# Performance work log

Hardware: AMD Instinct MI355X
Metric: run time of the kernel (lower is better)

Reference implementation:

```python
import jax, jax.numpy as jnp
import numpy as np

# Module hyperparameters (init_kwargs)
THRESHOLD_ABS = 0.2
THRESHOLD_REL = 0.05   # set to None to disable the relative-threshold branch
MIN_DISTANCE = 3


def setup_inputs() -> dict:
    key = jax.random.key(0)
    # belief maps in [0, 1), NCHW
    belive_map = jax.random.uniform(key, (32, 4, 512, 512), dtype=jnp.float32)
    return {"belive_map": belive_map}


def reference(belive_map):
    """Peak detection on belief maps (dense, jit-friendly form).

    Faithful to BeliveMapsNMS.forward: the torch module additionally compacts
    the mask into (coords, labels, scores) lists via nonzero/gather, which has
    data-dependent shapes; here we return the equivalent dense outputs:
      mask        [B,C,H,W] bool   - peak locations (nonzero of this == torch ind)
      scores_abs  [B,C,H,W] f32    - belief value at peaks, 0 elsewhere
      scores_rel  [B,C,H,W] f32    - scores_abs / per-(b,c) max
    """
    k = 2 * MIN_DISTANCE + 1          # 7
    pad = k // 2                       # 3 -> 'same' max pool, stride 1

    # F.max_pool2d(kernel=k, stride=1, padding=k//2)
    x_max = jax.lax.reduce_window(
        belive_map, -jnp.inf, jax.lax.max,
        window_dimensions=(1, 1, k, k),
        window_strides=(1, 1, 1, 1),
        padding=[(0, 0), (0, 0), (pad, pad), (pad, pad)],
    )

    # per-(batch, channel) global max: hh.max(dim=2) on the flattened map
    vmax = jnp.max(belive_map, axis=(2, 3), keepdims=True)  # [B,C,1,1]

    mask = (x_max == belive_map) & (belive_map > THRESHOLD_ABS)
    if THRESHOLD_REL is not None:
        mask = mask & (belive_map > THRESHOLD_REL * vmax)

    scores_abs = jnp.where(mask, belive_map, jnp.float32(0.0))
    scores_rel = scores_abs / vmax
    return mask, scores_abs, scores_rel
```

## Files before the change

### kernel.cpp

```cpp
#include <hip/hip_runtime.h>
#include <math.h>


#define H 512
#define W 512
#define PLANE_ELEMS (H * W)
#define TH 8
#define LROWS (TH + 6)
#define NEG_INF (-INFINITY)
#define VCHUNKS 16

typedef float v4f __attribute__((ext_vector_type(4)));

__device__ __forceinline__ float4 vmax4(float4 a, float4 b) {
    return make_float4(fmaxf(a.x, b.x), fmaxf(a.y, b.y), fmaxf(a.z, b.z), fmaxf(a.w, b.w));
}

__device__ __forceinline__ void nt_store4(float* p, float a, float b, float c, float d) {
    v4f v = {a, b, c, d};
    __builtin_nontemporal_store(v, (v4f*)p);
}

__global__ __launch_bounds__(256) void vmax_kernel(const float* __restrict__ in,
                                                   float* __restrict__ partials) {
    const int chunk = blockIdx.x;
    const int plane = blockIdx.y;
    const float4* p = (const float4*)(in + (size_t)plane * PLANE_ELEMS) + chunk * 4096;
    float4 v[16];
    #pragma unroll
    for (int j = 0; j < 16; ++j) v[j] = p[threadIdx.x + (j << 8)];
    float4 t[8];
    #pragma unroll
    for (int j = 0; j < 8; ++j) t[j] = vmax4(v[j], v[j + 8]);
    #pragma unroll
    for (int j = 0; j < 4; ++j) t[j] = vmax4(t[j], t[j + 4]);
    float4 q = vmax4(vmax4(t[0], t[1]), vmax4(t[2], t[3]));
    float m = fmaxf(fmaxf(q.x, q.y), fmaxf(q.z, q.w));
    #pragma unroll
    for (int o = 32; o > 0; o >>= 1) m = fmaxf(m, __shfl_down(m, o, 64));
    __shared__ float s[4];
    if ((threadIdx.x & 63) == 0) s[threadIdx.x >> 6] = m;
    __syncthreads();
    if (threadIdx.x == 0) {
        partials[(plane << 4) + chunk] = fmaxf(fmaxf(s[0], s[1]), fmaxf(s[2], s[3]));
    }
}

__global__ __launch_bounds__(256, 4) void nms_kernel(const float* __restrict__ in,
                                                     const float* __restrict__ partials,
                                                     float* __restrict__ out, int N) {
    const int hwid = blockIdx.x + (blockIdx.y << 6);
    const int wg = ((hwid & 7) << 10) + (hwid >> 3);
    const int plane = wg >> 6;
    const int ty0 = (wg & 63) * TH;

    const float* pin = in + (size_t)plane * PLANE_ELEMS;

    __shared__ __align__(16) float sRow[LROWS * W];

    const int wid = threadIdx.x >> 6;
    const int lane = threadIdx.x & 63;
    const int c8 = lane << 3;

    float pm[16];
    #pragma unroll
    for (int j = 0; j < 16; ++j) pm[j] = partials[(plane << 4) + j];

    float4 va[4], vb[4];
    #pragma unroll
    for (int k = 0; k < 4; ++k) {
        const int r = wid + (k << 2);
        if (r < LROWS) {
            const int gy = ty0 + r - 3;
            if (gy >= 0 && gy < H) {
                const float4* row = (const float4*)(pin + (size_t)gy * W);
                va[k] = row[lane * 2];
                vb[k] = row[lane * 2 + 1];
            } else {
                va[k] = vb[k] = make_float4(NEG_INF, NEG_INF, NEG_INF, NEG_INF);
            }
        }
    }

    #pragma unroll
    for (int k = 0; k < 4; ++k) {
        const int r = wid + (k << 2);
        if (r < LROWS) {
            float4 v0 = va[k], v1 = vb[k];
            float l0 = __shfl_up(v1.y, 1, 64), l1 = __shfl_up(v1.z, 1, 64), l2 = __shfl_up(v1.w, 1, 64);
            float r0 = __shfl_down(v0.x, 1, 64), r1 = __shfl_down(v0.y, 1, 64), r2 = __shfl_down(v0.z, 1, 64);
            if (lane == 0) { l0 = NEG_INF; l1 = NEG_INF; l2 = NEG_INF; }
            if (lane == 63) { r0 = NEG_INF; r1 = NEG_INF; r2 = NEG_INF; }
            float a[14] = {l0, l1, l2, v0.x, v0.y, v0.z, v0.w, v1.x, v1.y, v1.z, v1.w, r0, r1, r2};
            float A[7];
            A[6] = a[6];
            #pragma unroll
            for (int j = 5; j >= 0; --j) A[j] = fmaxf(a[j], A[j + 1]);
            float rm[8];
            rm[0] = A[0];
            float B = a[7];
            rm[1] = fmaxf(A[1], B);
            #pragma unroll
            for (int j = 2; j <= 6; ++j) { B = fmaxf(B, a[6 + j]); rm[j] = fmaxf(A[j], B); }
            B = fmaxf(B, a[13]);
            rm[7] = B;
            float4* dst = (float4*)&sRow[r * W + c8];
            dst[0] = make_float4(rm[0], rm[1], rm[2], rm[3]);
            dst[1] = make_float4(rm[4], rm[5], rm[6], rm[7]);
        }
    }

    const int strip = threadIdx.x >> 7;
    const int cg = threadIdx.x & 127;
    const int c = cg << 2;
    const int y0 = strip << 2;
    const int gy_base = ty0 + y0;

    float4 ctr[4];
    #pragma unroll
    for (int i = 0; i < 4; ++i) {
        ctr[i] = *(const float4*)(pin + (size_t)(gy_base + i) * W + c);
    }

    float vmax = pm[0];
    #pragma unroll
    for (int j = 1; j < 16; ++j) vmax = fmaxf(vmax, pm[j]);
    const float rel_thr = 0.05f * vmax;
    const float inv_vmax = 1.0f / vmax;

    __syncthreads();

    float* __restrict__ omask = out;
    float* __restrict__ oabs = out + (size_t)N;
    float* __restrict__ orel = out + 2 * (size_t)N;

    float4 Lr[7];
    #pragma unroll
    for (int k = 0; k < 7; ++k) Lr[k] = *(const float4*)&sRow[(y0 + k) * W + c];
    float4 Aq[4];
    {
        float4 suf = vmax4(Lr[4], vmax4(Lr[5], Lr[6]));
        Aq[3] = vmax4(Lr[3], suf);
        Aq[2] = vmax4(Lr[2], Aq[3]);
        Aq[1] = vmax4(Lr[1], Aq[2]);
        Aq[0] = vmax4(Lr[0], Aq[1]);
    }

    float4 Bq;
    #pragma unroll
    for (int i = 0; i < 4; ++i) {
        float4 m;
        if (i == 0) {
            m = Aq[0];
        } else {
            float4 row = *(const float4*)&sRow[(y0 + 6 + i) * W + c];
            Bq = (i == 1) ? row : vmax4(Bq, row);
            m = vmax4(Aq[i], Bq);
        }
        const int gy = gy_base + i;
        const float4 cc = ctr[i];
        const bool p0 = (m.x == cc.x) & (cc.x > 0.2f) & (cc.x > rel_thr);
        const bool p1 = (m.y == cc.y) & (cc.y > 0.2f) & (cc.y > rel_thr);
        const bool p2 = (m.z == cc.z) & (cc.z > 0.2f) & (cc.z > rel_thr);
        const bool p3 = (m.w == cc.w) & (cc.w > 0.2f) & (cc.w > rel_thr);
        const float a0 = p0 ? cc.x : 0.0f, a1 = p1 ? cc.y : 0.0f;
        const float a2 = p2 ? cc.z : 0.0f, a3 = p3 ? cc.w : 0.0f;
        const size_t o = (size_t)plane * PLANE_ELEMS + (size_t)gy * W + c;
        nt_store4(omask + o, p0 ? 1.0f : 0.0f, p1 ? 1.0f : 0.0f,
                             p2 ? 1.0f : 0.0f, p3 ? 1.0f : 0.0f);
        nt_store4(oabs + o, a0, a1, a2, a3);
        nt_store4(orel + o, a0 * inv_vmax, a1 * inv_vmax, a2 * inv_vmax, a3 * inv_vmax);
    }
}

extern "C" void kernel_launch(void* const* d_in, const int* in_sizes, int n_in,
                              void* d_out, int out_size, void* d_ws, size_t ws_size,
                              hipStream_t stream) {
    const float* in = (const float*)d_in[0];
    float* out = (float*)d_out;
    const int N = in_sizes[0];
    const int planes = N / PLANE_ELEMS;

    float* partials = (float*)d_ws;

    vmax_kernel<<<dim3(VCHUNKS, planes), 256, 0, stream>>>(in, partials);
    nms_kernel<<<dim3(H / TH, planes), 256, 0, stream>>>(in, partials, out, N);
}
```

Measured before the change: 477.1 us.

## Do vertical max in registers first, then horizontal max via shared memory

Reorders the separable 7x7 max pool so each thread loads a 14-row column slab of float4s directly from global memory and computes the vertical 7-row max in registers. Only the column-max results go to a padded shared buffer, which is then read for the horizontal pass. The tile height doubles to 16 rows, so the 6-row halo is reloaded less often, and the centre values now come from the loaded registers instead of a second global read. In exchange each thread holds many more live float4 registers, which may limit occupancy under the 4-blocks launch bound, and the grid shrinks to half as many blocks.

```diff
diff --git a/kernel.cpp b/kernel.cpp
--- a/kernel.cpp
+++ b/kernel.cpp
@@ -5,8 +5,9 @@
 #define H 512
 #define W 512
 #define PLANE_ELEMS (H * W)
-#define TH 8
-#define LROWS (TH + 6)
+#define TH 16
+#define NROWS 14
+#define RW 520
 #define NEG_INF (-INFINITY)
 #define VCHUNKS 16
 
@@ -49,82 +50,63 @@
 __global__ __launch_bounds__(256, 4) void nms_kernel(const float* __restrict__ in,
                                                      const float* __restrict__ partials,
                                                      float* __restrict__ out, int N) {
-    const int hwid = blockIdx.x + (blockIdx.y << 6);
-    const int wg = ((hwid & 7) << 10) + (hwid >> 3);
-    const int plane = wg >> 6;
-    const int ty0 = (wg & 63) * TH;
+    const int hwid = blockIdx.x + (blockIdx.y << 5);
+    const int wg = ((hwid & 7) << 9) + (hwid >> 3);
+    const int plane = wg >> 5;
+    const int ty0 = (wg & 31) * TH;
 
     const float* pin = in + (size_t)plane * PLANE_ELEMS;
 
-    __shared__ __align__(16) float sRow[LROWS * W];
+    __shared__ __align__(16) float sCol[TH * RW];
 
-    const int wid = threadIdx.x >> 6;
-    const int lane = threadIdx.x & 63;
-    const int c8 = lane << 3;
+    const int cg = threadIdx.x & 127;
+    const int strip = threadIdx.x >> 7;
+    const int c = cg << 2;
+    const int y0 = strip << 3;
+    const int gy0 = ty0 + y0;
 
-    float pm[16];
+    float4 r[NROWS];
     #pragma unroll
-    for (int j = 0; j < 16; ++j) pm[j] = partials[(plane << 4) + j];
-
-    float4 va[4], vb[4];
-    #pragma unroll
-    for (int k = 0; k < 4; ++k) {
-        const int r = wid + (k << 2);
-        if (r < LROWS) {
-            const int gy = ty0 + r - 3;
-            if (gy >= 0 && gy < H) {
-                const float4* row = (const float4*)(pin + (size_t)gy * W);
-                va[k] = row[lane * 2];
-                vb[k] = row[lane * 2 + 1];
-            } else {
-                va[k] = vb[k] = make_float4(NEG_INF, NEG_INF, NEG_INF, NEG_INF);
-            }
+    for (int k = 0; k < NROWS; ++k) {
+        const int gy = gy0 + k - 3;
+        if (gy >= 0 && gy < H) {
+            r[k] = *(const float4*)(pin + (size_t)gy * W + c);
+        } else {
+            r[k] = make_float4(NEG_INF, NEG_INF, NEG_INF, NEG_INF);
         }
     }
 
+    float4 A[7];
+    A[6] = r[6];
     #pragma unroll
-    for (int k = 0; k < 4; ++k) {
-        const int r = wid + (k << 2);
-        if (r < LROWS) {
-            float4 v0 = va[k], v1 = vb[k];
-            float l0 = __shfl_up(v1.y, 1, 64), l1 = __shfl_up(v1.z, 1, 64), l2 = __shfl_up(v1.w, 1, 64);
-            float r0 = __shfl_down(v0.x, 1, 64), r1 = __shfl_down(v0.y, 1, 64), r2 = __shfl_down(v0.z, 1, 64);
-            if (lane == 0) { l0 = NEG_INF; l1 = NEG_INF; l2 = NEG_INF; }
-            if (lane == 63) { r0 = NEG_INF; r1 = NEG_INF; r2 = NEG_INF; }
-            float a[14] = {l0, l1, l2, v0.x, v0.y, v0.z, v0.w, v1.x, v1.y, v1.z, v1.w, r0, r1, r2};
-            float A[7];
-            A[6] = a[6];
-            #pragma unroll
-            for (int j = 5; j >= 0; --j) A[j] = fmaxf(a[j], A[j + 1]);
-            float rm[8];
-            rm[0] = A[0];
-            float B = a[7];
-            rm[1] = fmaxf(A[1], B);
-            #pragma unroll
-            for (int j = 2; j <= 6; ++j) { B = fmaxf(B, a[6 + j]); rm[j] = fmaxf(A[j], B); }
-            B = fmaxf(B, a[13]);
-            rm[7] = B;
-            float4* dst = (float4*)&sRow[r * W + c8];
-            dst[0] = make_float4(rm[0], rm[1], rm[2], rm[3]);
-            dst[1] = make_float4(rm[4], rm[5], rm[6], rm[7]);
-        }
+    for (int j = 5; j >= 0; --j) A[j] = vmax4(r[j], A[j + 1]);
+    float4 cm[8];
+    cm[0] = A[0];
+    float4 Bv = r[7];
+    cm[1] = vmax4(A[1], Bv);
+    #pragma unroll
+    for (int j = 2; j <= 6; ++j) { Bv = vmax4(Bv, r[j + 6]); cm[j] = vmax4(A[j], Bv); }
+    Bv = vmax4(Bv, r[13]);
+    cm[7] = Bv;
+
+    #pragma unroll
+    for (int i = 0; i < 8; ++i) {
+        *(float4*)&sCol[(y0 + i) * RW + 4 + c] = cm[i];
+    }
+    if (threadIdx.x < TH) {
+        *(float4*)&sCol[threadIdx.x * RW] =
+            make_float4(NEG_INF, NEG_INF, NEG_INF, NEG_INF);
+    } else if (threadIdx.x < 2 * TH) {
+        *(float4*)&sCol[(threadIdx.x - TH) * RW + 4 + W] =
+            make_float4(NEG_INF, NEG_INF, NEG_INF, NEG_INF);
     }
 
-    const int strip = threadIdx.x >> 7;
-    const int cg = threadIdx.x & 127;
-    const int c = cg << 2;
-    const int y0 = strip << 2;
-    const int gy_base = ty0 + y0;
-
-    float4 ctr[4];
-    #pragma unroll
-    for (int i = 0; i < 4; ++i) {
-        ctr[i] = *(const float4*)(pin + (size_t)(gy_base + i) * W + c);
-    }
-
-    float vmax = pm[0];
-    #pragma unroll
-    for (int j = 1; j < 16; ++j) vmax = fmaxf(vmax, pm[j]);
+    float4 pm0 = *(const float4*)&partials[(plane << 4) + 0];
+    float4 pm1 = *(const float4*)&partials[(plane << 4) + 4];
+    float4 pm2 = *(const float4*)&partials[(plane << 4) + 8];
+    float4 pm3 = *(const float4*)&partials[(plane << 4) + 12];
+    float4 q = vmax4(vmax4(pm0, pm1), vmax4(pm2, pm3));
+    const float vmax = fmaxf(fmaxf(q.x, q.y), fmaxf(q.z, q.w));
     const float rel_thr = 0.05f * vmax;
     const float inv_vmax = 1.0f / vmax;
 
@@ -134,42 +116,36 @@
     float* __restrict__ oabs = out + (size_t)N;
     float* __restrict__ orel = out + 2 * (size_t)N;
 
-    float4 Lr[7];
     #pragma unroll
-    for (int k = 0; k < 7; ++k) Lr[k] = *(const float4*)&sRow[(y0 + k) * W + c];
-    float4 Aq[4];
-    {
-        float4 suf = vmax4(Lr[4], vmax4(Lr[5], Lr[6]));
-        Aq[3] = vmax4(Lr[3], suf);
-        Aq[2] = vmax4(Lr[2], Aq[3]);
-        Aq[1] = vmax4(Lr[1], Aq[2]);
-        Aq[0] = vmax4(Lr[0], Aq[1]);
-    }
+    for (int i = 0; i < 8; ++i) {
+        const int rowb = (y0 + i) * RW;
+        const float4 lo = *(const float4*)&sCol[rowb + c];
+        const float4 hi = *(const float4*)&sCol[rowb + c + 8];
+        const float a0 = lo.y, a1 = lo.z, a2 = lo.w;
+        const float a3 = cm[i].x, a4 = cm[i].y, a5 = cm[i].z, a6 = cm[i].w;
+        const float a7 = hi.x, a8 = hi.y, a9 = hi.z;
+        const float t5 = fmaxf(a5, a6), t4 = fmaxf(a4, t5), t3 = fmaxf(a3, t4);
+        const float t2 = fmaxf(a2, t3), t1 = fmaxf(a1, t2), t0 = fmaxf(a0, t1);
+        const float b2 = fmaxf(a7, a8), b3 = fmaxf(b2, a9);
+        const float m0 = t0;
+        const float m1 = fmaxf(t1, a7);
+        const float m2 = fmaxf(t2, b2);
+        const float m3 = fmaxf(t3, b3);
 
-    float4 Bq;
-    #pragma unroll
-    for (int i = 0; i < 4; ++i) {
-        float4 m;
-        if (i == 0) {
-            m = Aq[0];
-        } else {
-            float4 row = *(const float4*)&sRow[(y0 + 6 + i) * W + c];
-            Bq = (i == 1) ? row : vmax4(Bq, row);
-            m = vmax4(Aq[i], Bq);
-        }
-        const int gy = gy_base + i;
-        const float4 cc = ctr[i];
-        const bool p0 = (m.x == cc.x) & (cc.x > 0.2f) & (cc.x > rel_thr);
-        const bool p1 = (m.y == cc.y) & (cc.y > 0.2f) & (cc.y > rel_thr);
-        const bool p2 = (m.z == cc.z) & (cc.z > 0.2f) & (cc.z > rel_thr);
-        const bool p3 = (m.w == cc.w) & (cc.w > 0.2f) & (cc.w > rel_thr);
-        const float a0 = p0 ? cc.x : 0.0f, a1 = p1 ? cc.y : 0.0f;
-        const float a2 = p2 ? cc.z : 0.0f, a3 = p3 ? cc.w : 0.0f;
+        const float4 cc = r[i + 3];
+        const bool p0 = (m0 == cc.x) & (cc.x > 0.2f) & (cc.x > rel_thr);
+        const bool p1 = (m1 == cc.y) & (cc.y > 0.2f) & (cc.y > rel_thr);
+        const bool p2 = (m2 == cc.z) & (cc.z > 0.2f) & (cc.z > rel_thr);
+        const bool p3 = (m3 == cc.w) & (cc.w > 0.2f) & (cc.w > rel_thr);
+        const float a0s = p0 ? cc.x : 0.0f, a1s = p1 ? cc.y : 0.0f;
+        const float a2s = p2 ? cc.z : 0.0f, a3s = p3 ? cc.w : 0.0f;
+        const int gy = gy0 + i;
         const size_t o = (size_t)plane * PLANE_ELEMS + (size_t)gy * W + c;
         nt_store4(omask + o, p0 ? 1.0f : 0.0f, p1 ? 1.0f : 0.0f,
                              p2 ? 1.0f : 0.0f, p3 ? 1.0f : 0.0f);
-        nt_store4(oabs + o, a0, a1, a2, a3);
-        nt_store4(orel + o, a0 * inv_vmax, a1 * inv_vmax, a2 * inv_vmax, a3 * inv_vmax);
+        nt_store4(oabs + o, a0s, a1s, a2s, a3s);
+        nt_store4(orel + o, a0s * inv_vmax, a1s * inv_vmax,
+                            a2s * inv_vmax, a3s * inv_vmax);
     }
 }
 
```

After: 482.7 us. No clear change (+1.2%).
